# Kernel optimization log

Hardware: AMD Instinct MI355X
Metric: run time of the kernel (lower is better)

Reference implementation:

```python
import jax, jax.numpy as jnp
import numpy as np

B, S, M = 4, 4096, 2048
LATENT, H, D = 512, 16, 128  # latent_dim, num_heads, hidden_dim (per-head)


def setup_inputs() -> dict:
    key = jax.random.key(0)
    ks = jax.random.split(key, 12)
    sd = lambda fan_in: 1.0 / np.sqrt(fan_in)
    return {
        "x": jax.random.normal(ks[0], (B, S, M), dtype=jnp.float32),
        # k path: down-proj to latent, up-proj to H*D (vmapped Dense pair, slice 0)
        "Wd_k": jax.random.normal(ks[1], (M, LATENT), dtype=jnp.float32) * sd(M),
        "bd_k": jnp.zeros((LATENT,), dtype=jnp.float32),
        "Wu_k": jax.random.normal(ks[2], (LATENT, H * D), dtype=jnp.float32) * sd(LATENT),
        "bu_k": jnp.zeros((H * D,), dtype=jnp.float32),
        # v path (slice 1 of the vmapped params)
        "Wd_v": jax.random.normal(ks[3], (M, LATENT), dtype=jnp.float32) * sd(M),
        "bd_v": jnp.zeros((LATENT,), dtype=jnp.float32),
        "Wu_v": jax.random.normal(ks[4], (LATENT, H * D), dtype=jnp.float32) * sd(LATENT),
        "bu_v": jnp.zeros((H * D,), dtype=jnp.float32),
        # q projection
        "Wq": jax.random.normal(ks[5], (M, H * D), dtype=jnp.float32) * sd(M),
        "bq": jnp.zeros((H * D,), dtype=jnp.float32),
        # output projection
        "Wo": jax.random.normal(ks[6], (H * D, M), dtype=jnp.float32) * sd(H * D),
        "bo": jnp.zeros((M,), dtype=jnp.float32),
    }


def reference(x, Wd_k, bd_k, Wu_k, bu_k, Wd_v, bd_v, Wu_v, bu_v, Wq, bq, Wo, bo):
    b, s, m = x.shape
    # low-rank KV: down-project to latent cache, up-project to heads
    cache_k = x @ Wd_k + bd_k                      # [B,S,L]
    cache_v = x @ Wd_v + bd_v                      # [B,S,L]
    k = (cache_k @ Wu_k + bu_k).reshape(b, s, H, D)
    v = (cache_v @ Wu_v + bu_v).reshape(b, s, H, D)
    q = (x @ Wq + bq).reshape(b, s, H, D)
    # NOTE: source permutes k as (0,1,3,2) on [B,S,H,D] -> scores are per-token
    # head-vs-head [B,S,H,H], softmax over the last (head) axis.
    sim = jnp.einsum("bshd,bsgd->bshg", q, k) * (D ** -0.5)
    attn = jax.nn.softmax(sim, axis=-1)            # [B,S,H,H]
    out = jnp.einsum("bshg,bsgd->bshd", attn, v)   # [B,S,H,D]
    out = out.reshape(b, s, H * D)
    return out @ Wo + bo                           # [B,S,M]
```

## Files before the change

kernel.cpp:

```cpp
#include <hip/hip_runtime.h>

typedef __attribute__((ext_vector_type(8))) short short8v;
typedef __attribute__((ext_vector_type(4))) float f32x4;
typedef __attribute__((ext_vector_type(4))) unsigned int uint4v;

#define GLOBAL_AS(p) ((const __attribute__((address_space(1))) void*)(p))
#define LDS_AS(p)    ((__attribute__((address_space(3))) void*)(p))
#define WAITV(n) asm volatile("s_waitcnt vmcnt(" #n ")" ::: "memory")
#define BARRIER() __builtin_amdgcn_s_barrier()
#define SCHED0() __builtin_amdgcn_sched_barrier(0)

__device__ __forceinline__ unsigned short f2bf(float f) {
  unsigned int u = __builtin_bit_cast(unsigned int, f);
  u += 0x7fffu + ((u >> 16) & 1u);
  return (unsigned short)(u >> 16);
}
__device__ __forceinline__ float bf2f(unsigned short u) {
  unsigned int x = ((unsigned int)u) << 16;
  return __builtin_bit_cast(float, x);
}

__global__ __launch_bounds__(256) void transpose_to_bf16(
    const float* __restrict__ src, unsigned short* __restrict__ dst,
    int K, int N, int ntx) {
  __shared__ float tile[32][33];
  const int bx = blockIdx.x % ntx;
  const int by = blockIdx.x / ntx;
  const int tx = threadIdx.x & 31, ty = threadIdx.x >> 5;
  const int k0 = by * 32, n0 = bx * 32;
#pragma unroll
  for (int i = 0; i < 32; i += 8)
    tile[ty + i][tx] = src[(size_t)(k0 + ty + i) * N + n0 + tx];
  __syncthreads();
#pragma unroll
  for (int i = 0; i < 32; i += 8)
    dst[(size_t)(n0 + ty + i) * K + k0 + tx] = f2bf(tile[tx][ty + i]);
}

__global__ __launch_bounds__(256) void cvt_f32_bf16(
    const float* __restrict__ s, unsigned short* __restrict__ d) {
  size_t i = ((size_t)blockIdx.x * 256 + threadIdx.x) * 8;
  f32x4 v0 = *(const f32x4*)(s + i);
  f32x4 v1 = *(const f32x4*)(s + i + 4);
  union U8 { uint4v v; unsigned short us[8]; } o;
  o.us[0] = f2bf(v0.x); o.us[1] = f2bf(v0.y); o.us[2] = f2bf(v0.z); o.us[3] = f2bf(v0.w);
  o.us[4] = f2bf(v1.x); o.us[5] = f2bf(v1.y); o.us[6] = f2bf(v1.z); o.us[7] = f2bf(v1.w);
  *(uint4v*)(d + i) = o.v;
}

__global__ __launch_bounds__(256) void fill_bias(
    const float* __restrict__ bd_k, const float* __restrict__ bd_v,
    const float* __restrict__ bq, const float* __restrict__ bu_k,
    const float* __restrict__ bu_v, float* __restrict__ b1, float* __restrict__ b2) {
  int i = blockIdx.x * 256 + threadIdx.x;
  if (i < 512) b1[i] = bd_k[i];
  else if (i < 1024) b1[i] = bd_v[i - 512];
  else if (i < 3072) b1[i] = bq[i - 1024];
  else if (i < 5120) b2[i - 3072] = bu_k[i - 3072];
  else if (i < 7168) b2[i - 3072] = bu_v[i - 5120];
}

template <int OUT_BF16>
__global__ __launch_bounds__(512, 2) void gemm_bt(
    const unsigned short* __restrict__ A, int lda, int nsplit_col, int acol_off,
    const unsigned short* __restrict__ Bt, int ldb,
    const float* __restrict__ bias, void* __restrict__ Cp, int ldc,
    int K, int ntn) {
  __shared__ unsigned short lds[2][2][256 * 64];
  const int t = threadIdx.x;
  const int lane = t & 63, wave = t >> 6;

  const int q = gridDim.x >> 3;
  const int bid = (blockIdx.x & 7) * q + (blockIdx.x >> 3);
  const int bm = (bid / ntn) * 256;
  const int bn = (bid % ntn) * 256;
  const unsigned short* Ab = A + (bn >= nsplit_col ? acol_off : 0);

  const int wr = wave >> 2, wc = wave & 3;
  const int g = lane >> 4, r = lane & 15;
  const int srow = t >> 3, sj = t & 7;
  const int jsrc = sj ^ (srow & 7);
  const int NT = K >> 6;

  f32x4 acc[8][4];
#pragma unroll
  for (int i = 0; i < 8; ++i)
#pragma unroll
    for (int j = 0; j < 4; ++j) acc[i][j] = (f32x4){0.f, 0.f, 0.f, 0.f};

  const unsigned short* aptr = Ab + (size_t)(bm + srow) * lda + (jsrc << 3);
  const unsigned short* bptr = Bt + (size_t)(bn + srow) * ldb + (jsrc << 3);
  const int sbase = wave * 512;

  auto stage = [&](int kt, int buf) {
    const unsigned short* ak = aptr + kt * 64;
    const unsigned short* bk = bptr + kt * 64;
    unsigned short* la = &lds[buf][0][sbase];
    unsigned short* lb = &lds[buf][1][sbase];
#pragma unroll
    for (int c = 0; c < 4; ++c) {
      __builtin_amdgcn_global_load_lds(GLOBAL_AS(ak + (size_t)c * 64 * lda),
                                       LDS_AS(la + c * 4096), 16, 0, 0);
      __builtin_amdgcn_global_load_lds(GLOBAL_AS(bk + (size_t)c * 64 * ldb),
                                       LDS_AS(lb + c * 4096), 16, 0, 0);
    }
  };

  stage(0, 0);

  const int arow = wr * 128 + r;
  const int brow = wc * 64 + r;
  const int swz = r & 7;

  for (int kt = 0; kt < NT; ++kt) {
    const int cur = kt & 1;
    if (kt + 1 < NT) {
      stage(kt + 1, cur ^ 1);
      SCHED0();
      WAITV(8);
    } else {
      WAITV(0);
    }
    BARRIER();
    SCHED0();
    const unsigned short* la = lds[cur][0];
    const unsigned short* lb = lds[cur][1];
#pragma unroll
    for (int ks = 0; ks < 2; ++ks) {
      const int c16 = (((ks << 2) + g) ^ swz) << 3;
      short8v bfr[4], afr[8];
#pragma unroll
      for (int ni = 0; ni < 4; ++ni)
        bfr[ni] = *(const short8v*)&lb[(brow + ni * 16) * 64 + c16];
#pragma unroll
      for (int mi = 0; mi < 8; ++mi)
        afr[mi] = *(const short8v*)&la[(arow + mi * 16) * 64 + c16];
      __builtin_amdgcn_s_setprio(1);
#pragma unroll
      for (int mi = 0; mi < 8; ++mi)
#pragma unroll
        for (int ni = 0; ni < 4; ++ni)
          acc[mi][ni] = __builtin_amdgcn_mfma_f32_16x16x32_bf16(
              afr[mi], bfr[ni], acc[mi][ni], 0, 0, 0);
      __builtin_amdgcn_s_setprio(0);
    }
    SCHED0();
    BARRIER();
    SCHED0();
  }

#pragma unroll
  for (int ni = 0; ni < 4; ++ni) {
    const int col = bn + wc * 64 + ni * 16 + r;
    const float bv = bias[col];
#pragma unroll
    for (int mi = 0; mi < 8; ++mi) {
      const int row0 = bm + wr * 128 + mi * 16 + (g << 2);
#pragma unroll
      for (int j = 0; j < 4; ++j) {
        float v = acc[mi][ni][j] + bv;
        if (OUT_BF16)
          ((unsigned short*)Cp)[(size_t)(row0 + j) * ldc + col] = f2bf(v);
        else
          ((float*)Cp)[(size_t)(row0 + j) * ldc + col] = v;
      }
    }
  }
}

__global__ __launch_bounds__(256) void attn_kernel(
    const unsigned short* __restrict__ out1, const unsigned short* __restrict__ kv,
    unsigned short* __restrict__ aout) {
  const int s = blockIdx.x;
  const int t = threadIdx.x;
  __shared__ float qs[16 * 132], ks2[16 * 132], vs[16 * 132];
  __shared__ float attn[256];
  const int h = t >> 4, d0 = (t & 15) * 8;

  union U8 { uint4v v; unsigned short us[8]; };
  U8 qv, kv8, vv;
  qv.v = *(const uint4v*)(out1 + (size_t)s * 3072 + 1024 + t * 8);
  kv8.v = *(const uint4v*)(kv + (size_t)s * 4096 + t * 8);
  vv.v = *(const uint4v*)(kv + (size_t)s * 4096 + 2048 + t * 8);
#pragma unroll
  for (int j = 0; j < 8; ++j) {
    qs[h * 132 + d0 + j] = bf2f(qv.us[j]);
    ks2[h * 132 + d0 + j] = bf2f(kv8.us[j]);
    vs[h * 132 + d0 + j] = bf2f(vv.us[j]);
  }
  __syncthreads();

  const int gg0 = t & 15;
  const f32x4* qrow = (const f32x4*)&qs[h * 132];
  const f32x4* krow = (const f32x4*)&ks2[gg0 * 132];
  float acc = 0.f;
#pragma unroll
  for (int dd = 0; dd < 32; ++dd) {
    f32x4 a4 = qrow[dd], b4 = krow[dd];
    acc += a4.x * b4.x + a4.y * b4.y + a4.z * b4.z + a4.w * b4.w;
  }
  acc *= 0.08838834764831845f;
  float mx = acc;
#pragma unroll
  for (int o = 8; o; o >>= 1) mx = fmaxf(mx, __shfl_xor(mx, o));
  float e = __expf(acc - mx);
  float sm = e;
#pragma unroll
  for (int o = 8; o; o >>= 1) sm += __shfl_xor(sm, o);
  attn[t] = e / sm;
  __syncthreads();

  f32x4 o0 = (f32x4){0.f, 0.f, 0.f, 0.f}, o1 = (f32x4){0.f, 0.f, 0.f, 0.f};
#pragma unroll
  for (int gg = 0; gg < 16; ++gg) {
    const float a = attn[(h << 4) + gg];
    f32x4 v0 = *(const f32x4*)&vs[gg * 132 + d0];
    f32x4 v1 = *(const f32x4*)&vs[gg * 132 + d0 + 4];
    o0 += v0 * a;
    o1 += v1 * a;
  }
  U8 ov;
  ov.us[0] = f2bf(o0.x); ov.us[1] = f2bf(o0.y); ov.us[2] = f2bf(o0.z); ov.us[3] = f2bf(o0.w);
  ov.us[4] = f2bf(o1.x); ov.us[5] = f2bf(o1.y); ov.us[6] = f2bf(o1.z); ov.us[7] = f2bf(o1.w);
  *(uint4v*)(aout + (size_t)s * 2048 + t * 8) = ov.v;
}

extern "C" void kernel_launch(void* const* d_in, const int* in_sizes, int n_in,
                              void* d_out, int out_size, void* d_ws, size_t ws_size,
                              hipStream_t stream) {
  (void)in_sizes; (void)n_in; (void)out_size; (void)ws_size;
  const float* x    = (const float*)d_in[0];
  const float* Wd_k = (const float*)d_in[1];
  const float* bd_k = (const float*)d_in[2];
  const float* Wu_k = (const float*)d_in[3];
  const float* bu_k = (const float*)d_in[4];
  const float* Wd_v = (const float*)d_in[5];
  const float* bd_v = (const float*)d_in[6];
  const float* Wu_v = (const float*)d_in[7];
  const float* bu_v = (const float*)d_in[8];
  const float* Wq   = (const float*)d_in[9];
  const float* bq   = (const float*)d_in[10];
  const float* Wo   = (const float*)d_in[11];
  const float* bo   = (const float*)d_in[12];

  char* ws = (char*)d_ws;
  unsigned short* w1t  = (unsigned short*)(ws);
  unsigned short* w2t  = (unsigned short*)(ws + 12582912);
  unsigned short* w3t  = (unsigned short*)(ws + 16777216);
  float*          b1   = (float*)(ws + 25165824);
  float*          b2   = (float*)(ws + 25178112);
  unsigned short* xb   = (unsigned short*)(ws + 25194496);
  unsigned short* out1 = (unsigned short*)(ws + 92303360);
  unsigned short* kvb  = (unsigned short*)(ws + 192966656);
  unsigned short* attO = xb;

  dim3 blk(256);

  transpose_to_bf16<<<dim3(16 * 64), blk, 0, stream>>>(Wd_k, w1t,               2048, 512, 16);
  transpose_to_bf16<<<dim3(16 * 64), blk, 0, stream>>>(Wd_v, w1t + 512 * 2048,  2048, 512, 16);
  transpose_to_bf16<<<dim3(64 * 64), blk, 0, stream>>>(Wq,   w1t + 1024 * 2048, 2048, 2048, 64);
  transpose_to_bf16<<<dim3(64 * 16), blk, 0, stream>>>(Wu_k, w2t,               512, 2048, 64);
  transpose_to_bf16<<<dim3(64 * 16), blk, 0, stream>>>(Wu_v, w2t + 2048 * 512,  512, 2048, 64);
  transpose_to_bf16<<<dim3(64 * 64), blk, 0, stream>>>(Wo,   w3t,               2048, 2048, 64);

  fill_bias<<<dim3(28), blk, 0, stream>>>(bd_k, bd_v, bq, bu_k, bu_v, b1, b2);

  cvt_f32_bf16<<<dim3(16384), blk, 0, stream>>>(x, xb);

  gemm_bt<1><<<dim3(64 * 12), dim3(512), 0, stream>>>(
      xb, 2048, 1 << 30, 0, w1t, 2048, b1, out1, 3072, 2048, 12);

  gemm_bt<1><<<dim3(64 * 16), dim3(512), 0, stream>>>(
      out1, 3072, 2048, 512, w2t, 512, b2, kvb, 4096, 512, 16);

  attn_kernel<<<dim3(16384), blk, 0, stream>>>(out1, kvb, attO);

  gemm_bt<0><<<dim3(64 * 8), dim3(512), 0, stream>>>(
      attO, 2048, 1 << 30, 0, w3t, 2048, bo, (float*)d_out, 2048, 2048, 8);
}
```

Baseline: 609.3 us.

## Split GEMM k-tile into four phases interleaving LDS reads, MFMAs and staged loads

Restructures the bf16 GEMM main loop so each 64-wide k-tile is processed in four sub-phases, two M-halves by two k-steps. Each sub-phase reads a smaller set of LDS fragments and runs a quarter of the MFMAs. Global-to-LDS loads for the next tile, and A quarters for the tile after next, are issued between phases as soon as the matching buffer region is free. The aim is to overlap memory traffic with MFMA work more finely and to lower register pressure from fragment arrays. The cost is more barriers and lgkmcnt waits per iteration, plus fragile vmcnt accounting.

```diff
diff --git a/kernel.cpp b/kernel.cpp
--- a/kernel.cpp
+++ b/kernel.cpp
@@ -7,6 +7,7 @@
 #define GLOBAL_AS(p) ((const __attribute__((address_space(1))) void*)(p))
 #define LDS_AS(p)    ((__attribute__((address_space(3))) void*)(p))
 #define WAITV(n) asm volatile("s_waitcnt vmcnt(" #n ")" ::: "memory")
+#define LGKM0()  asm volatile("s_waitcnt lgkmcnt(0)" ::: "memory")
 #define BARRIER() __builtin_amdgcn_s_barrier()
 #define SCHED0() __builtin_amdgcn_sched_barrier(0)
 
@@ -70,16 +71,15 @@
   const int t = threadIdx.x;
   const int lane = t & 63, wave = t >> 6;
 
-  const int q = gridDim.x >> 3;
-  const int bid = (blockIdx.x & 7) * q + (blockIdx.x >> 3);
+  const int qx = gridDim.x >> 3;
+  const int bid = (blockIdx.x & 7) * qx + (blockIdx.x >> 3);
   const int bm = (bid / ntn) * 256;
   const int bn = (bid % ntn) * 256;
   const unsigned short* Ab = A + (bn >= nsplit_col ? acol_off : 0);
 
   const int wr = wave >> 2, wc = wave & 3;
   const int g = lane >> 4, r = lane & 15;
-  const int srow = t >> 3, sj = t & 7;
-  const int jsrc = sj ^ (srow & 7);
+  const int swz = r & 7;
   const int NT = K >> 6;
 
   f32x4 acc[8][4];
@@ -88,65 +88,102 @@
 #pragma unroll
     for (int j = 0; j < 4; ++j) acc[i][j] = (f32x4){0.f, 0.f, 0.f, 0.f};
 
-  const unsigned short* aptr = Ab + (size_t)(bm + srow) * lda + (jsrc << 3);
-  const unsigned short* bptr = Bt + (size_t)(bn + srow) * ldb + (jsrc << 3);
-  const int sbase = wave * 512;
-
-  auto stage = [&](int kt, int buf) {
-    const unsigned short* ak = aptr + kt * 64;
-    const unsigned short* bk = bptr + kt * 64;
-    unsigned short* la = &lds[buf][0][sbase];
-    unsigned short* lb = &lds[buf][1][sbase];
-#pragma unroll
-    for (int c = 0; c < 4; ++c) {
-      __builtin_amdgcn_global_load_lds(GLOBAL_AS(ak + (size_t)c * 64 * lda),
-                                       LDS_AS(la + c * 4096), 16, 0, 0);
-      __builtin_amdgcn_global_load_lds(GLOBAL_AS(bk + (size_t)c * 64 * ldb),
-                                       LDS_AS(lb + c * 4096), 16, 0, 0);
-    }
+  const int trow = t >> 3;
+  const int jsrc = (t & 7) ^ (trow & 7);
+  const unsigned short* aptr = Ab + (size_t)(bm + trow) * lda + (jsrc << 3);
+  const unsigned short* bptr = Bt + (size_t)(bn + trow) * ldb + (jsrc << 3);
+  const int wbase = wave * 512;
+
+  auto stageA = [&](int kt, int buf, int q64) {
+    __builtin_amdgcn_global_load_lds(
+        GLOBAL_AS(aptr + (size_t)(q64 * 64) * lda + kt * 64),
+        LDS_AS(&lds[buf][0][q64 * 4096 + wbase]), 16, 0, 0);
   };
-
-  stage(0, 0);
-
-  const int arow = wr * 128 + r;
-  const int brow = wc * 64 + r;
-  const int swz = r & 7;
-
-  for (int kt = 0; kt < NT; ++kt) {
-    const int cur = kt & 1;
-    if (kt + 1 < NT) {
-      stage(kt + 1, cur ^ 1);
-      SCHED0();
-      WAITV(8);
-    } else {
-      WAITV(0);
-    }
-    BARRIER();
-    SCHED0();
+  auto stageB = [&](int kt, int buf, int q64) {
+    __builtin_amdgcn_global_load_lds(
+        GLOBAL_AS(bptr + (size_t)(q64 * 64) * ldb + kt * 64),
+        LDS_AS(&lds[buf][1][q64 * 4096 + wbase]), 16, 0, 0);
+  };
+
+  auto phaseReads = [&](const unsigned short* la, const unsigned short* lb,
+                        int miH, int ks, short8v (&af)[4], short8v (&bf)[4]) {
+    const int c16 = (((ks << 2) + g) ^ swz) << 3;
+#pragma unroll
+    for (int mi = 0; mi < 4; ++mi)
+      af[mi] = *(const short8v*)&la[(wr * 128 + miH * 64 + mi * 16 + r) * 64 + c16];
+#pragma unroll
+    for (int ni = 0; ni < 4; ++ni)
+      bf[ni] = *(const short8v*)&lb[(wc * 64 + ni * 16 + r) * 64 + c16];
+  };
+  auto phaseMfma = [&](int miH, short8v (&af)[4], short8v (&bf)[4]) {
+    __builtin_amdgcn_s_setprio(1);
+#pragma unroll
+    for (int mi = 0; mi < 4; ++mi)
+#pragma unroll
+      for (int ni = 0; ni < 4; ++ni)
+        acc[miH * 4 + mi][ni] = __builtin_amdgcn_mfma_f32_16x16x32_bf16(
+            af[mi], bf[ni], acc[miH * 4 + mi][ni], 0, 0, 0);
+    __builtin_amdgcn_s_setprio(0);
+  };
+
+  stageA(0, 0, 0); stageA(0, 0, 1); stageA(0, 0, 2); stageA(0, 0, 3);
+  stageB(0, 0, 0); stageB(0, 0, 1); stageB(0, 0, 2); stageB(0, 0, 3);
+  if (NT > 1) { stageA(1, 1, 0); stageA(1, 1, 2); }
+  WAITV(2);
+  BARRIER();
+
+  for (int T = 0; T < NT; ++T) {
+    const int cur = T & 1, nxt = cur ^ 1;
     const unsigned short* la = lds[cur][0];
     const unsigned short* lb = lds[cur][1];
-#pragma unroll
-    for (int ks = 0; ks < 2; ++ks) {
-      const int c16 = (((ks << 2) + g) ^ swz) << 3;
-      short8v bfr[4], afr[8];
-#pragma unroll
-      for (int ni = 0; ni < 4; ++ni)
-        bfr[ni] = *(const short8v*)&lb[(brow + ni * 16) * 64 + c16];
-#pragma unroll
-      for (int mi = 0; mi < 8; ++mi)
-        afr[mi] = *(const short8v*)&la[(arow + mi * 16) * 64 + c16];
-      __builtin_amdgcn_s_setprio(1);
-#pragma unroll
-      for (int mi = 0; mi < 8; ++mi)
-#pragma unroll
-        for (int ni = 0; ni < 4; ++ni)
-          acc[mi][ni] = __builtin_amdgcn_mfma_f32_16x16x32_bf16(
-              afr[mi], bfr[ni], acc[mi][ni], 0, 0, 0);
-      __builtin_amdgcn_s_setprio(0);
+    const bool s1 = (T + 1 < NT), s2 = (T + 2 < NT);
+    short8v af[4], bf[4];
+
+    SCHED0();
+    phaseReads(la, lb, 0, 0, af, bf);
+    SCHED0();
+    if (s1) {
+      stageA(T + 1, nxt, 1); stageA(T + 1, nxt, 3);
+      stageB(T + 1, nxt, 0); stageB(T + 1, nxt, 1);
     }
     SCHED0();
     BARRIER();
-    SCHED0();
+    LGKM0(); SCHED0();
+    phaseMfma(0, af, bf);
+    SCHED0();
+    BARRIER();
+
+    SCHED0();
+    phaseReads(la, lb, 0, 1, af, bf);
+    SCHED0();
+    if (s1) { stageB(T + 1, nxt, 2); stageB(T + 1, nxt, 3); }
+    SCHED0();
+    BARRIER();
+    LGKM0(); SCHED0();
+    phaseMfma(0, af, bf);
+    SCHED0();
+    BARRIER();
+
+    SCHED0();
+    phaseReads(la, lb, 1, 0, af, bf);
+    SCHED0();
+    if (s2) { stageA(T + 2, cur, 0); stageA(T + 2, cur, 2); }
+    SCHED0();
+    BARRIER();
+    LGKM0(); SCHED0();
+    phaseMfma(1, af, bf);
+    SCHED0();
+    BARRIER();
+
+    SCHED0();
+    phaseReads(la, lb, 1, 1, af, bf);
+    SCHED0();
+    BARRIER();
+    LGKM0(); SCHED0();
+    phaseMfma(1, af, bf);
+    SCHED0();
+    if (s2) { WAITV(2); } else { WAITV(0); }
+    BARRIER();
   }
 
 #pragma unroll
```

Measured after the change: 620.9 us. Within noise of the previous version (+1.9%).

## Deepen GEMM pipeline to 4-stage K=32 ring with register double-buffered fragments

Applied to the files above, without the earlier changes.

Replaces the 2-buffer K=64 LDS pipeline in the bf16 GEMM with a 4-slot ring of K=32 tiles, keeping three stages of global-to-LDS loads in flight. LDS fragments for the next K-step are read into a second register set while MFMAs run on the current set, so LDS reads overlap math. Sched barriers are removed and the swizzle is changed to suit 32-wide rows. This costs more registers for the double fragment sets and more barriers per unit of K, which could lower occupancy under the 512-thread, 2-block launch bounds.

```diff
diff --git a/kernel.cpp b/kernel.cpp
--- a/kernel.cpp
+++ b/kernel.cpp
@@ -8,7 +8,6 @@
 #define LDS_AS(p)    ((__attribute__((address_space(3))) void*)(p))
 #define WAITV(n) asm volatile("s_waitcnt vmcnt(" #n ")" ::: "memory")
 #define BARRIER() __builtin_amdgcn_s_barrier()
-#define SCHED0() __builtin_amdgcn_sched_barrier(0)
 
 __device__ __forceinline__ unsigned short f2bf(float f) {
   unsigned int u = __builtin_bit_cast(unsigned int, f);
@@ -66,21 +65,21 @@
     const unsigned short* __restrict__ Bt, int ldb,
     const float* __restrict__ bias, void* __restrict__ Cp, int ldc,
     int K, int ntn) {
-  __shared__ unsigned short lds[2][2][256 * 64];
+  __shared__ unsigned short lds[4][2][256 * 32];
   const int t = threadIdx.x;
   const int lane = t & 63, wave = t >> 6;
 
-  const int q = gridDim.x >> 3;
-  const int bid = (blockIdx.x & 7) * q + (blockIdx.x >> 3);
+  const int qx = gridDim.x >> 3;
+  const int bid = (blockIdx.x & 7) * qx + (blockIdx.x >> 3);
   const int bm = (bid / ntn) * 256;
   const int bn = (bid % ntn) * 256;
   const unsigned short* Ab = A + (bn >= nsplit_col ? acol_off : 0);
 
   const int wr = wave >> 2, wc = wave & 3;
   const int g = lane >> 4, r = lane & 15;
-  const int srow = t >> 3, sj = t & 7;
-  const int jsrc = sj ^ (srow & 7);
-  const int NT = K >> 6;
+  const int swz = r & 3;
+  const int cchunk = (g ^ swz) << 3;
+  const int NT = K >> 5;
 
   f32x4 acc[8][4];
 #pragma unroll
@@ -88,65 +87,66 @@
 #pragma unroll
     for (int j = 0; j < 4; ++j) acc[i][j] = (f32x4){0.f, 0.f, 0.f, 0.f};
 
+  const int srow = t >> 2;
+  const int jsrc = (t & 3) ^ (srow & 3);
   const unsigned short* aptr = Ab + (size_t)(bm + srow) * lda + (jsrc << 3);
   const unsigned short* bptr = Bt + (size_t)(bn + srow) * ldb + (jsrc << 3);
-  const int sbase = wave * 512;
-
-  auto stage = [&](int kt, int buf) {
-    const unsigned short* ak = aptr + kt * 64;
-    const unsigned short* bk = bptr + kt * 64;
-    unsigned short* la = &lds[buf][0][sbase];
-    unsigned short* lb = &lds[buf][1][sbase];
-#pragma unroll
-    for (int c = 0; c < 4; ++c) {
-      __builtin_amdgcn_global_load_lds(GLOBAL_AS(ak + (size_t)c * 64 * lda),
-                                       LDS_AS(la + c * 4096), 16, 0, 0);
-      __builtin_amdgcn_global_load_lds(GLOBAL_AS(bk + (size_t)c * 64 * ldb),
-                                       LDS_AS(lb + c * 4096), 16, 0, 0);
+  const int wbase = wave * 512;
+
+  auto stage = [&](int kt) {
+    const int buf = kt & 3;
+    const unsigned short* ak = aptr + kt * 32;
+    const unsigned short* bk = bptr + kt * 32;
+    unsigned short* la = &lds[buf][0][wbase];
+    unsigned short* lb = &lds[buf][1][wbase];
+#pragma unroll
+    for (int u = 0; u < 2; ++u) {
+      __builtin_amdgcn_global_load_lds(GLOBAL_AS(ak + (size_t)(u * 128) * lda),
+                                       LDS_AS(la + u * 4096), 16, 0, 0);
+      __builtin_amdgcn_global_load_lds(GLOBAL_AS(bk + (size_t)(u * 128) * ldb),
+                                       LDS_AS(lb + u * 4096), 16, 0, 0);
     }
   };
 
-  stage(0, 0);
-
-  const int arow = wr * 128 + r;
-  const int brow = wc * 64 + r;
-  const int swz = r & 7;
-
-  for (int kt = 0; kt < NT; ++kt) {
-    const int cur = kt & 1;
-    if (kt + 1 < NT) {
-      stage(kt + 1, cur ^ 1);
-      SCHED0();
-      WAITV(8);
-    } else {
-      WAITV(0);
-    }
+  auto readFrags = [&](int kt, short8v (&af)[8], short8v (&bf)[4]) {
+    const unsigned short* la = lds[kt & 3][0];
+    const unsigned short* lb = lds[kt & 3][1];
+#pragma unroll
+    for (int mi = 0; mi < 8; ++mi)
+      af[mi] = *(const short8v*)&la[(wr * 128 + mi * 16 + r) * 32 + cchunk];
+#pragma unroll
+    for (int ni = 0; ni < 4; ++ni)
+      bf[ni] = *(const short8v*)&lb[(wc * 64 + ni * 16 + r) * 32 + cchunk];
+  };
+
+  auto mfma32 = [&](short8v (&af)[8], short8v (&bf)[4]) {
+    __builtin_amdgcn_s_setprio(1);
+#pragma unroll
+    for (int mi = 0; mi < 8; ++mi)
+#pragma unroll
+      for (int ni = 0; ni < 4; ++ni)
+        acc[mi][ni] = __builtin_amdgcn_mfma_f32_16x16x32_bf16(
+            af[mi], bf[ni], acc[mi][ni], 0, 0, 0);
+    __builtin_amdgcn_s_setprio(0);
+  };
+
+  stage(0); stage(1); stage(2);
+  WAITV(8);
+  BARRIER();
+  short8v afA[8], bfA[4], afB[8], bfB[4];
+  readFrags(0, afA, bfA);
+
+  for (int T = 0; T < NT; T += 2) {
+    if (T + 2 < NT) { WAITV(4); } else { WAITV(0); }
     BARRIER();
-    SCHED0();
-    const unsigned short* la = lds[cur][0];
-    const unsigned short* lb = lds[cur][1];
-#pragma unroll
-    for (int ks = 0; ks < 2; ++ks) {
-      const int c16 = (((ks << 2) + g) ^ swz) << 3;
-      short8v bfr[4], afr[8];
-#pragma unroll
-      for (int ni = 0; ni < 4; ++ni)
-        bfr[ni] = *(const short8v*)&lb[(brow + ni * 16) * 64 + c16];
-#pragma unroll
-      for (int mi = 0; mi < 8; ++mi)
-        afr[mi] = *(const short8v*)&la[(arow + mi * 16) * 64 + c16];
-      __builtin_amdgcn_s_setprio(1);
-#pragma unroll
-      for (int mi = 0; mi < 8; ++mi)
-#pragma unroll
-        for (int ni = 0; ni < 4; ++ni)
-          acc[mi][ni] = __builtin_amdgcn_mfma_f32_16x16x32_bf16(
-              afr[mi], bfr[ni], acc[mi][ni], 0, 0, 0);
-      __builtin_amdgcn_s_setprio(0);
-    }
-    SCHED0();
+    if (T + 3 < NT) stage(T + 3);
+    readFrags(T + 1, afB, bfB);
+    mfma32(afA, bfA);
+    if (T + 3 < NT) { WAITV(4); } else { WAITV(0); }
     BARRIER();
-    SCHED0();
+    if (T + 4 < NT) stage(T + 4);
+    if (T + 2 < NT) readFrags(T + 2, afA, bfA);
+    mfma32(afB, bfB);
   }
 
 #pragma unroll
```

Measured after the change: 626.2 us. 2.8% more time.

## Restructure GEMM to 256x128 tiles with B fragments loaded directly to registers

Applied to the files above, without the earlier changes.

The bf16 GEMM kernel moves from 512-thread 256x256 tiles, where both A and B are staged through LDS, to 256-thread 256x128 tiles. Only A is staged in LDS via global_load_lds. Each wave loads its B fragments straight from global memory into registers, using a two-deep manually unrolled double buffer. The block-to-tile mapping now walks M-tiles first (ntm=64), and the grids double. This halves LDS use and removes the B LDS round-trip, but B reads are no longer shared across waves, which adds global/L2 traffic, and each tile now reuses data less.

```diff
diff --git a/kernel.cpp b/kernel.cpp
--- a/kernel.cpp
+++ b/kernel.cpp
@@ -8,7 +8,6 @@
 #define LDS_AS(p)    ((__attribute__((address_space(3))) void*)(p))
 #define WAITV(n) asm volatile("s_waitcnt vmcnt(" #n ")" ::: "memory")
 #define BARRIER() __builtin_amdgcn_s_barrier()
-#define SCHED0() __builtin_amdgcn_sched_barrier(0)
 
 __device__ __forceinline__ unsigned short f2bf(float f) {
   unsigned int u = __builtin_bit_cast(unsigned int, f);
@@ -61,25 +60,23 @@
 }
 
 template <int OUT_BF16>
-__global__ __launch_bounds__(512, 2) void gemm_bt(
+__global__ __launch_bounds__(256, 2) void gemm_bt(
     const unsigned short* __restrict__ A, int lda, int nsplit_col, int acol_off,
     const unsigned short* __restrict__ Bt, int ldb,
     const float* __restrict__ bias, void* __restrict__ Cp, int ldc,
-    int K, int ntn) {
-  __shared__ unsigned short lds[2][2][256 * 64];
+    int K, int ntm) {
+  __shared__ unsigned short Als[2][256 * 64];
   const int t = threadIdx.x;
   const int lane = t & 63, wave = t >> 6;
 
-  const int q = gridDim.x >> 3;
-  const int bid = (blockIdx.x & 7) * q + (blockIdx.x >> 3);
-  const int bm = (bid / ntn) * 256;
-  const int bn = (bid % ntn) * 256;
+  const int qx = gridDim.x >> 3;
+  const int bid = (blockIdx.x & 7) * qx + (blockIdx.x >> 3);
+  const int bm = (bid % ntm) * 256;
+  const int bn = (bid / ntm) * 128;
   const unsigned short* Ab = A + (bn >= nsplit_col ? acol_off : 0);
 
-  const int wr = wave >> 2, wc = wave & 3;
+  const int wr = wave >> 1, wc = wave & 1;
   const int g = lane >> 4, r = lane & 15;
-  const int srow = t >> 3, sj = t & 7;
-  const int jsrc = sj ^ (srow & 7);
   const int NT = K >> 6;
 
   f32x4 acc[8][4];
@@ -88,65 +85,59 @@
 #pragma unroll
     for (int j = 0; j < 4; ++j) acc[i][j] = (f32x4){0.f, 0.f, 0.f, 0.f};
 
+  const int srow = t >> 3;
+  const int jsrc = (t & 7) ^ (srow & 7);
   const unsigned short* aptr = Ab + (size_t)(bm + srow) * lda + (jsrc << 3);
-  const unsigned short* bptr = Bt + (size_t)(bn + srow) * ldb + (jsrc << 3);
-  const int sbase = wave * 512;
 
   auto stage = [&](int kt, int buf) {
-    const unsigned short* ak = aptr + kt * 64;
-    const unsigned short* bk = bptr + kt * 64;
-    unsigned short* la = &lds[buf][0][sbase];
-    unsigned short* lb = &lds[buf][1][sbase];
-#pragma unroll
-    for (int c = 0; c < 4; ++c) {
-      __builtin_amdgcn_global_load_lds(GLOBAL_AS(ak + (size_t)c * 64 * lda),
-                                       LDS_AS(la + c * 4096), 16, 0, 0);
-      __builtin_amdgcn_global_load_lds(GLOBAL_AS(bk + (size_t)c * 64 * ldb),
-                                       LDS_AS(lb + c * 4096), 16, 0, 0);
+    const unsigned short* ak = aptr + (size_t)kt * 64;
+    unsigned short* ld = &Als[buf][wave * 512];
+#pragma unroll
+    for (int u = 0; u < 8; ++u)
+      __builtin_amdgcn_global_load_lds(GLOBAL_AS(ak + (size_t)(u * 32) * lda),
+                                       LDS_AS(ld + u * 2048), 16, 0, 0);
+  };
+
+  const unsigned short* bptr = Bt + (size_t)(bn + wc * 64 + r) * ldb + (g << 3);
+  auto loadB = [&](short8v (&bx)[4][2], int kt) {
+    const unsigned short* p = bptr + (size_t)kt * 64;
+#pragma unroll
+    for (int ni = 0; ni < 4; ++ni)
+#pragma unroll
+      for (int ks = 0; ks < 2; ++ks)
+        bx[ni][ks] = *(const short8v*)(p + (size_t)ni * 16 * ldb + ks * 32);
+  };
+
+  auto compute = [&](int buf, short8v (&bx)[4][2]) {
+#pragma unroll
+    for (int ks = 0; ks < 2; ++ks) {
+      const int c16 = (((ks << 2) + g) ^ (r & 7)) << 3;
+      __builtin_amdgcn_s_setprio(1);
+#pragma unroll
+      for (int mi = 0; mi < 8; ++mi) {
+        short8v af = *(const short8v*)&Als[buf][(wr * 128 + mi * 16 + r) * 64 + c16];
+#pragma unroll
+        for (int ni = 0; ni < 4; ++ni)
+          acc[mi][ni] = __builtin_amdgcn_mfma_f32_16x16x32_bf16(
+              af, bx[ni][ks], acc[mi][ni], 0, 0, 0);
+      }
+      __builtin_amdgcn_s_setprio(0);
     }
   };
 
+  short8v bA[4][2], bB[4][2];
   stage(0, 0);
-
-  const int arow = wr * 128 + r;
-  const int brow = wc * 64 + r;
-  const int swz = r & 7;
-
-  for (int kt = 0; kt < NT; ++kt) {
-    const int cur = kt & 1;
-    if (kt + 1 < NT) {
-      stage(kt + 1, cur ^ 1);
-      SCHED0();
-      WAITV(8);
-    } else {
-      WAITV(0);
-    }
+  loadB(bA, 0);
+
+  for (int T = 0; T < NT; T += 2) {
+    if (T + 1 < NT) { stage(T + 1, 1); loadB(bB, T + 1); WAITV(16); }
+    else { WAITV(0); }
     BARRIER();
-    SCHED0();
-    const unsigned short* la = lds[cur][0];
-    const unsigned short* lb = lds[cur][1];
-#pragma unroll
-    for (int ks = 0; ks < 2; ++ks) {
-      const int c16 = (((ks << 2) + g) ^ swz) << 3;
-      short8v bfr[4], afr[8];
-#pragma unroll
-      for (int ni = 0; ni < 4; ++ni)
-        bfr[ni] = *(const short8v*)&lb[(brow + ni * 16) * 64 + c16];
-#pragma unroll
-      for (int mi = 0; mi < 8; ++mi)
-        afr[mi] = *(const short8v*)&la[(arow + mi * 16) * 64 + c16];
-      __builtin_amdgcn_s_setprio(1);
-#pragma unroll
-      for (int mi = 0; mi < 8; ++mi)
-#pragma unroll
-        for (int ni = 0; ni < 4; ++ni)
-          acc[mi][ni] = __builtin_amdgcn_mfma_f32_16x16x32_bf16(
-              afr[mi], bfr[ni], acc[mi][ni], 0, 0, 0);
-      __builtin_amdgcn_s_setprio(0);
-    }
-    SCHED0();
+    compute(0, bA);
+    if (T + 2 < NT) { stage(T + 2, 0); loadB(bA, T + 2); WAITV(16); }
+    else { WAITV(0); }
     BARRIER();
-    SCHED0();
+    compute(1, bB);
   }
 
 #pragma unroll
@@ -267,14 +258,14 @@
 
   cvt_f32_bf16<<<dim3(16384), blk, 0, stream>>>(x, xb);
 
-  gemm_bt<1><<<dim3(64 * 12), dim3(512), 0, stream>>>(
-      xb, 2048, 1 << 30, 0, w1t, 2048, b1, out1, 3072, 2048, 12);
-
-  gemm_bt<1><<<dim3(64 * 16), dim3(512), 0, stream>>>(
-      out1, 3072, 2048, 512, w2t, 512, b2, kvb, 4096, 512, 16);
+  gemm_bt<1><<<dim3(64 * 24), blk, 0, stream>>>(
+      xb, 2048, 1 << 30, 0, w1t, 2048, b1, out1, 3072, 2048, 64);
+
+  gemm_bt<1><<<dim3(64 * 32), blk, 0, stream>>>(
+      out1, 3072, 2048, 512, w2t, 512, b2, kvb, 4096, 512, 64);
 
   attn_kernel<<<dim3(16384), blk, 0, stream>>>(out1, kvb, attO);
 
-  gemm_bt<0><<<dim3(64 * 8), dim3(512), 0, stream>>>(
-      attO, 2048, 1 << 30, 0, w3t, 2048, bo, (float*)d_out, 2048, 2048, 8);
-}
+  gemm_bt<0><<<dim3(64 * 16), blk, 0, stream>>>(
+      attO, 2048, 1 << 30, 0, w3t, 2048, bo, (float*)d_out, 2048, 2048, 64);
+}
```

Measured after the change: 1.655 ms. +171.6%, slower.
